# Kernel optimization log

Measured on AMD Instinct MI355X. Metric: run time of the kernel, lower is better.

## Reference

```python
import jax, jax.numpy as jnp
import numpy as np

D_MODEL = 192; D_INNER = 384; N_STATE = 16; D_CONV = 4; DT_RANK = 12; DEPTH = 24
PATCH = 16; STRIDE = 16; IMG = 128; EPS = 1e-5


def _ln(x, w, b):
    m = jnp.mean(x, -1, keepdims=True)
    v = jnp.mean((x - m) ** 2, -1, keepdims=True)
    return (x - m) * jax.lax.rsqrt(v + EPS) * w + b


def _mamba_dir(xz, cw, cb, xpw, dpw, dpb, Alog, Dv):
    # xz: (B, L, 2*d_inner); one direction of the bidirectional Mamba mixer
    xp, z = jnp.split(xz, 2, axis=-1)               # (B,L,di) each
    xc = jnp.transpose(xp, (0, 2, 1))               # (B,di,L)
    xc = jnp.pad(xc, ((0, 0), (0, 0), (D_CONV - 1, 0)))  # causal pad
    xc = jax.lax.conv_general_dilated(
        xc, cw, (1,), 'VALID',
        dimension_numbers=('NCH', 'OIH', 'NCH'),
        feature_group_count=D_INNER) + cb[None, :, None]
    u = jax.nn.silu(jnp.transpose(xc, (0, 2, 1)))   # (B,L,di)
    dbl = u @ xpw.T                                  # (B,L,dt_rank+2N)
    dt, Bm, Cm = jnp.split(dbl, [DT_RANK, DT_RANK + N_STATE], axis=-1)
    dt = jax.nn.softplus(dt @ dpw.T + dpb)           # (B,L,di)
    A = -jnp.exp(Alog)                               # (di,N)
    dA = jnp.exp(dt[..., None] * A)                  # (B,L,di,N)
    dBu = (dt * u)[..., None] * Bm[:, :, None, :]    # (B,L,di,N)

    def comb(c1, c2):
        a1, b1 = c1
        a2, b2 = c2
        return a1 * a2, a2 * b1 + b2

    _, h = jax.lax.associative_scan(comb, (dA, dBu), axis=1)
    y = jnp.einsum('bldn,bln->bld', h, Cm) + u * Dv
    return y * jax.nn.silu(z)


def _forward(x, patch_w, patch_b, ln_w, ln_b, in_w,
             cf_w, cf_b, xpf_w, dtf_w, dtf_b, Alog_f, D_f,
             cbk_w, cbk_b, xpb_w, dtb_w, dtb_b, Alog_b, D_b,
             out_w, nf_w, nf_b, head_w, head_b):
    B = x.shape[0]
    p = jax.lax.conv_general_dilated(
        x, patch_w, (STRIDE,) * 3, 'VALID',
        dimension_numbers=('NCDHW', 'OIDHW', 'NCDHW')) + patch_b[None, :, None, None, None]
    hidden = p.reshape(B, D_MODEL, -1).transpose(0, 2, 1)  # (B, L=512, D)
    residual = jnp.zeros_like(hidden)

    xs = (ln_w, ln_b, in_w, cf_w, cf_b, xpf_w, dtf_w, dtf_b, Alog_f, D_f,
          cbk_w, cbk_b, xpb_w, dtb_w, dtb_b, Alog_b, D_b, out_w)

    def step(carry, pl):
        hidden, residual = carry
        (lw, lb, iw, cfw, cfb, xpf, dwf, dbf, Af, Dfv,
         cbw, cbb, xpb, dwb, dbb, Ab, Dbv, ow) = pl
        residual = residual + hidden
        hn = _ln(residual, lw, lb)
        xz = hn @ iw.T                               # (B,L,2di)
        yf = _mamba_dir(xz, cfw, cfb, xpf, dwf, dbf, Af, Dfv)
        yb = jnp.flip(_mamba_dir(jnp.flip(xz, 1), cbw, cbb, xpb, dwb, dbb, Ab, Dbv), 1)
        hidden = (yf + yb) @ ow.T
        return (hidden, residual), None

    (hidden, residual), _ = jax.lax.scan(step, (hidden, residual), xs)
    final = _ln(residual + hidden, nf_w, nf_b)
    feat = final[:, -1, :]                           # final_pool_type='none' -> last token
    return feat @ head_w.T + head_b


def setup_inputs() -> dict:
    key = jax.random.key(0)
    ks = jax.random.split(key, 16)
    rn = lambda k, s, sc=0.02: jax.random.normal(k, s, jnp.float32) * sc
    d = {}
    d['x'] = jax.random.normal(ks[0], (1, 1, IMG, IMG, IMG), jnp.float32)
    d['patch_w'] = rn(ks[1], (D_MODEL, 1, PATCH, PATCH, PATCH), 0.05)
    d['patch_b'] = jnp.zeros((D_MODEL,), jnp.float32)
    d['ln_w'] = jnp.ones((DEPTH, D_MODEL), jnp.float32)
    d['ln_b'] = jnp.zeros((DEPTH, D_MODEL), jnp.float32)
    d['in_w'] = rn(ks[2], (DEPTH, 2 * D_INNER, D_MODEL))
    d['cf_w'] = rn(ks[3], (DEPTH, D_INNER, 1, D_CONV), 0.2)
    d['cf_b'] = jnp.zeros((DEPTH, D_INNER), jnp.float32)
    d['xpf_w'] = rn(ks[4], (DEPTH, DT_RANK + 2 * N_STATE, D_INNER))
    d['dtf_w'] = rn(ks[5], (DEPTH, D_INNER, DT_RANK), 0.1)
    d['dtf_b'] = jnp.full((DEPTH, D_INNER), -4.6, jnp.float32)  # softplus -> dt~0.01
    d['Alog_f'] = jnp.log(jnp.broadcast_to(jnp.arange(1, N_STATE + 1, dtype=jnp.float32), (DEPTH, D_INNER, N_STATE)))
    d['D_f'] = jnp.ones((DEPTH, D_INNER), jnp.float32)
    d['cbk_w'] = rn(ks[6], (DEPTH, D_INNER, 1, D_CONV), 0.2)
    d['cbk_b'] = jnp.zeros((DEPTH, D_INNER), jnp.float32)
    d['xpb_w'] = rn(ks[7], (DEPTH, DT_RANK + 2 * N_STATE, D_INNER))
    d['dtb_w'] = rn(ks[8], (DEPTH, D_INNER, DT_RANK), 0.1)
    d['dtb_b'] = jnp.full((DEPTH, D_INNER), -4.6, jnp.float32)
    d['Alog_b'] = jnp.log(jnp.broadcast_to(jnp.arange(1, N_STATE + 1, dtype=jnp.float32), (DEPTH, D_INNER, N_STATE)))
    d['D_b'] = jnp.ones((DEPTH, D_INNER), jnp.float32)
    d['out_w'] = rn(ks[9], (DEPTH, D_MODEL, D_INNER))
    d['nf_w'] = jnp.ones((D_MODEL,), jnp.float32)
    d['nf_b'] = jnp.zeros((D_MODEL,), jnp.float32)
    d['head_w'] = rn(ks[10], (2, D_MODEL))
    d['head_b'] = jnp.zeros((2,), jnp.float32)
    return d


def reference(x, patch_w, patch_b, ln_w, ln_b, in_w,
              cf_w, cf_b, xpf_w, dtf_w, dtf_b, Alog_f, D_f,
              cbk_w, cbk_b, xpb_w, dtb_w, dtb_b, Alog_b, D_b,
              out_w, nf_w, nf_b, head_w, head_b):
    return _forward(x, patch_w, patch_b, ln_w, ln_b, in_w,
                    cf_w, cf_b, xpf_w, dtf_w, dtf_b, Alog_f, D_f,
                    cbk_w, cbk_b, xpb_w, dtb_w, dtb_b, Alog_b, D_b,
                    out_w, nf_w, nf_b, head_w, head_b)
```

## Files before the change

kernel.cpp:

```cpp
#include <hip/hip_runtime.h>
#include <hip/hip_bf16.h>

#define D_MODEL 192
#define D_INNER 384
#define N_STATE 16
#define DT_RANK 12
#define DEPTH 24
#define SEQ 512
#define NCHUNK 8
#define CLEN 64
#define TS 68
#define AS 33
#define PART_STRIDE (SEQ * D_MODEL)
#define USTR (SEQ * D_INNER)
#define KSPLIT 16
#define NBLK 512
#define FSTR 32

typedef __hip_bfloat16 bf16;
typedef unsigned short u16;
typedef unsigned long long u64;

__device__ __forceinline__ float silu_f(float x) { return x / (1.f + __expf(-x)); }
__device__ __forceinline__ float softplus_f(float x) {
    return (x > 20.f) ? x : log1pf(__expf(x));
}
__device__ __forceinline__ float bf2f(unsigned u) {
    return __uint_as_float(u << 16);
}
__device__ __forceinline__ u16 f2bu(float f) {
    bf16 b = __float2bfloat16(f);
    return *reinterpret_cast<u16*>(&b);
}

__device__ __forceinline__ float aload(const float* p) {
    return __hip_atomic_load(p, __ATOMIC_RELAXED, __HIP_MEMORY_SCOPE_AGENT);
}
__device__ __forceinline__ void astore(float* p, float v) {
    __hip_atomic_store(p, v, __ATOMIC_RELAXED, __HIP_MEMORY_SCOPE_AGENT);
}
__device__ __forceinline__ unsigned aloadu(const unsigned* p) {
    return __hip_atomic_load(p, __ATOMIC_RELAXED, __HIP_MEMORY_SCOPE_AGENT);
}
__device__ __forceinline__ void astoreu(unsigned* p, unsigned v) {
    __hip_atomic_store(p, v, __ATOMIC_RELAXED, __HIP_MEMORY_SCOPE_AGENT);
}
__device__ __forceinline__ float2 aload2(const float* p) {
    const u64 v = __hip_atomic_load((const u64*)p, __ATOMIC_RELAXED, __HIP_MEMORY_SCOPE_AGENT);
    return make_float2(__uint_as_float((unsigned)v), __uint_as_float((unsigned)(v >> 32)));
}
__device__ __forceinline__ void astore2(float* p, float x, float y) {
    const u64 v = (u64)__float_as_uint(x) | ((u64)__float_as_uint(y) << 32);
    __hip_atomic_store((u64*)p, v, __ATOMIC_RELAXED, __HIP_MEMORY_SCOPE_AGENT);
}
__device__ __forceinline__ float4 aload4v(const float* p) {
    const float2 a = aload2(p), b = aload2(p + 2);
    return make_float4(a.x, a.y, b.x, b.y);
}
__device__ __forceinline__ void astore4v(float* p, float4 v) {
    astore2(p, v.x, v.y); astore2(p + 2, v.z, v.w);
}

template<typename T> __device__ __forceinline__ float ld(const void* p, long i) {
    return ((const float*)p)[i];
}
template<> __device__ __forceinline__ float ld<bf16>(const void* p, long i) {
    return bf2f(((const u16*)p)[i]);
}
template<typename T> __device__ __forceinline__ float4 ld4(const void* p, long i) {
    return *(const float4*)((const float*)p + i);
}
template<> __device__ __forceinline__ float4 ld4<bf16>(const void* p, long i) {
    const ushort4 v = *(const ushort4*)((const u16*)p + i);
    return make_float4(bf2f(v.x), bf2f(v.y), bf2f(v.z), bf2f(v.w));
}
template<typename T> __device__ __forceinline__ void st(void* p, int i, float v) {
    ((float*)p)[i] = v;
}
template<> __device__ __forceinline__ void st<bf16>(void* p, int i, float v) {
    ((bf16*)p)[i] = __float2bfloat16(v);
}
__device__ __forceinline__ float dot4(const float4& a, const float4& b) {
    return a.x * b.x + a.y * b.y + a.z * b.z + a.w * b.w;
}
__device__ __forceinline__ void ld8b(const u16* p, float4& a, float4& b) {
    const uint4 u = *(const uint4*)p;
    a.x = bf2f(u.x & 0xffffu); a.y = bf2f(u.x >> 16);
    a.z = bf2f(u.y & 0xffffu); a.w = bf2f(u.y >> 16);
    b.x = bf2f(u.z & 0xffffu); b.y = bf2f(u.z >> 16);
    b.z = bf2f(u.w & 0xffffu); b.w = bf2f(u.w >> 16);
}
__device__ __forceinline__ float4 ld4b(const u16* p) {
    const uint2 u = *(const uint2*)p;
    return make_float4(bf2f(u.x & 0xffffu), bf2f(u.x >> 16),
                       bf2f(u.y & 0xffffu), bf2f(u.y >> 16));
}

__device__ __forceinline__ void gbar(unsigned* bar, unsigned target, bool fence) {
    asm volatile("s_waitcnt vmcnt(0)" ::: "memory");
    __syncthreads();
    const int bid = blockIdx.x, tid = threadIdx.x;
    unsigned* gen0 = bar + 512 * FSTR;
    if (tid == 0) {
        if (fence) __threadfence();
        astoreu(&bar[bid * FSTR], target);
    }
    if (bid == 0) {
        int spins = 0;
        for (;;) {
            const unsigned va = aloadu(&bar[tid * FSTR]);
            const unsigned vb = aloadu(&bar[(tid + 256) * FSTR]);
            const bool ok = (va >= target) && (vb >= target);
            if (__syncthreads_and(ok)) break;
            if (++spins > (1 << 20)) break;
            __builtin_amdgcn_s_sleep(1);
        }
        if (tid == 0) astoreu(gen0, target);
    } else if (tid == 0) {
        int spins = 0;
        if (bid < 16) {
            while (aloadu(gen0) < target) {
                if (++spins > (1 << 20)) break;
                __builtin_amdgcn_s_sleep(2);
            }
            astoreu(&gen0[bid * FSTR], target);
        } else if (bid < 32) {
            while (aloadu(gen0) < target) {
                if (++spins > (1 << 20)) break;
                __builtin_amdgcn_s_sleep(2);
            }
        } else {
            unsigned* rl = &gen0[(bid >> 5) * FSTR];
            while (aloadu(rl) < target) {
                if (++spins > (1 << 20)) break;
                __builtin_amdgcn_s_sleep(2);
            }
        }
    }
    if (fence && tid == 0) __threadfence();
    __syncthreads();
}

__device__ void cvtB(const void* s, u16* d, long n, long g, long str, int isb) {
    if (isb) {
        const u16* p = (const u16*)s;
        for (long i = g * 4; i < n; i += str * 4) *(ushort4*)(d + i) = *(const ushort4*)(p + i);
    } else {
        const float* p = (const float*)s;
        for (long i = g * 4; i < n; i += str * 4) {
            const float4 v = *(const float4*)(p + i);
            ushort4 o; o.x = f2bu(v.x); o.y = f2bu(v.y); o.z = f2bu(v.z); o.w = f2bu(v.w);
            *(ushort4*)(d + i) = o;
        }
    }
}
__device__ void cvtF(const void* s, float* d, long n, long g, long str, int isb) {
    if (isb) {
        const u16* p = (const u16*)s;
        for (long i = g * 4; i < n; i += str * 4) {
            const ushort4 v = *(const ushort4*)(p + i);
            *(float4*)(d + i) = make_float4(bf2f(v.x), bf2f(v.y), bf2f(v.z), bf2f(v.w));
        }
    } else {
        const float* p = (const float*)s;
        for (long i = g * 4; i < n; i += str * 4) *(float4*)(d + i) = *(const float4*)(p + i);
    }
}
__device__ void cvtNA(const void* s, float* d, long n, long g, long str, int isb) {
    if (isb) {
        const u16* p = (const u16*)s;
        for (long i = g * 4; i < n; i += str * 4) {
            const ushort4 v = *(const ushort4*)(p + i);
            *(float4*)(d + i) = make_float4(-__expf(bf2f(v.x)), -__expf(bf2f(v.y)),
                                            -__expf(bf2f(v.z)), -__expf(bf2f(v.w)));
        }
    } else {
        const float* p = (const float*)s;
        for (long i = g * 4; i < n; i += str * 4) {
            const float4 v = *(const float4*)(p + i);
            *(float4*)(d + i) = make_float4(-__expf(v.x), -__expf(v.y), -__expf(v.z), -__expf(v.w));
        }
    }
}

template<typename T>
__device__ void final_phase(int tid, const float* res, const float* y, const void* ow,
                            const void* nw, const void* nb, const void* hw, const void* hb,
                            void* out, float* syf, float* f, float* red) {
    for (int i = tid; i < D_INNER; i += 256)
        syf[i] = aload(&y[(long)511 * D_INNER + i]) + aload(&y[(long)USTR + 511 * D_INNER + i]);
    __syncthreads();
    float v = 0.f;
    if (tid < D_MODEL) {
        float acc = 0.f;
        const long wrow = (long)(DEPTH - 1) * D_MODEL * D_INNER + (long)tid * D_INNER;
        for (int k = 0; k < D_INNER; k += 4)
            acc += dot4(ld4<T>(ow, wrow + k), *(const float4*)&syf[k]);
        v = aload(&res[511 * D_MODEL + tid]) + acc;
    }
    float s = v;
    #pragma unroll
    for (int o = 32; o > 0; o >>= 1) s += __shfl_down(s, o, 64);
    if ((tid & 63) == 0 && tid < D_MODEL) red[tid >> 6] = s;
    __syncthreads();
    const float mean = (red[0] + red[1] + red[2]) * (1.f / D_MODEL);
    const float d = (tid < D_MODEL) ? (v - mean) : 0.f;
    float s2 = d * d;
    #pragma unroll
    for (int o = 32; o > 0; o >>= 1) s2 += __shfl_down(s2, o, 64);
    if ((tid & 63) == 0 && tid < D_MODEL) red[3 + (tid >> 6)] = s2;
    __syncthreads();
    const float var = (red[3] + red[4] + red[5]) * (1.f / D_MODEL);
    if (tid < D_MODEL)
        f[tid] = d * rsqrtf(var + 1e-5f) * ld<T>(nw, tid) + ld<T>(nb, tid);
    __syncthreads();
    if (tid < 2) {
        float a2 = ld<T>(hb, tid);
        for (int c = 0; c < D_MODEL; ++c) a2 += f[c] * ld<T>(hw, tid * D_MODEL + c);
        st<T>(out, tid, a2);
    }
}

struct MegaArgs {
    const void *x, *pw, *pb, *lnw, *lnb, *inw, *cfw, *cfb, *xpfw, *dtfw, *dtfb, *Af, *Dfv;
    const void *cbw, *cbb, *xpbw, *dtbw, *dtbb, *Ab, *Dbv, *ow, *nfw, *nfb, *hw, *hb;
    void* out;
    unsigned* bar;
    float *hidC, *res0, *res1, *xz, *u, *dbl, *dt, *y, *chunkH, *chunkP;
    float *lnwF, *lnbF, *cbfF, *cbbF, *dtbfF, *dtbbF, *negAfF, *negAbF, *DfF, *DbF, *pbF;
    u16 *inwB, *owB, *xB, *pwB, *xpwfB, *xpwbB, *dtwfB, *dtwbB, *cwfB, *cwbB;
};

__global__ void init_kernel(unsigned* bar) {
    const int i = blockIdx.x * 256 + threadIdx.x;
    ((uint4*)bar)[i] = make_uint4(0, 0, 0, 0);
}

__global__ void __launch_bounds__(256, 2) mega_kernel(MegaArgs a) {
    __shared__ float smem[6144];
    const int bid = blockIdx.x;
    const int tid = threadIdx.x;
    unsigned* bar = a.bar;
    unsigned* scanR = a.bar + 528 * FSTR;
    unsigned gen_ctr = 0;
    const int isb = (((const unsigned*)a.lnw)[0] != 0x3F800000u);

    {
        const long g = (long)bid * 256 + tid;
        const long str = (long)NBLK * 256;
        cvtB(a.inw,  a.inwB,  3538944, g, str, isb);
        cvtB(a.ow,   a.owB,   1769472, g, str, isb);
        cvtB(a.x,    a.xB,    2097152, g, str, isb);
        cvtB(a.pw,   a.pwB,    786432, g, str, isb);
        cvtB(a.xpfw, a.xpwfB,  405504, g, str, isb);
        cvtB(a.xpbw, a.xpwbB,  405504, g, str, isb);
        cvtB(a.dtfw, a.dtwfB,  110592, g, str, isb);
        cvtB(a.dtbw, a.dtwbB,  110592, g, str, isb);
        cvtB(a.cfw,  a.cwfB,    36864, g, str, isb);
        cvtB(a.cbw,  a.cwbB,    36864, g, str, isb);
        cvtF(a.lnw,  a.lnwF,     4608, g, str, isb);
        cvtF(a.lnb,  a.lnbF,     4608, g, str, isb);
        cvtF(a.cfb,  a.cbfF,     9216, g, str, isb);
        cvtF(a.cbb,  a.cbbF,     9216, g, str, isb);
        cvtF(a.dtfb, a.dtbfF,    9216, g, str, isb);
        cvtF(a.dtbb, a.dtbbF,    9216, g, str, isb);
        cvtF(a.pb,   a.pbF,       192, g, str, isb);
        cvtNA(a.Af,  a.negAfF,  147456, g, str, isb);
        cvtNA(a.Ab,  a.negAbF,  147456, g, str, isb);
        cvtF(a.Dfv,  a.DfF,      9216, g, str, isb);
        cvtF(a.Dbv,  a.DbF,      9216, g, str, isb);
    }
    gbar(bar, ++gen_ctr, true);

    {
        float* As_ = smem;
        float* Ws  = smem + 1056;
        const int ty = tid >> 4, tx = tid & 15;
        for (int unit = bid; unit < 768; unit += NBLK) {
            const int mt = unit & 15, nt = (unit >> 4) % 3, ks = unit / 48;
            const int m0 = mt * 32, n0 = nt * 64, kk0 = ks * 256;
            float acc[2][4] = {};
            for (int kk = kk0; kk < kk0 + 256; kk += 32) {
                for (int e = tid; e < 1024; e += 256) {
                    const int m = e >> 5, k = e & 31;
                    const int kid = kk + k, t = m0 + m;
                    const int dz = kid >> 8, dy = (kid >> 4) & 15, dx = kid & 15;
                    const int pz = t >> 6, py = (t >> 3) & 7, px = t & 7;
                    As_[k * AS + m] = bf2f(a.xB[(long)(pz * 16 + dz) * 16384 + (py * 16 + dy) * 128 + (px * 16 + dx)]);
                }
                for (int e = tid; e < 2048; e += 256) {
                    const int n = e >> 5, k = e & 31;
                    Ws[k * TS + n] = bf2f(a.pwB[(long)(n0 + n) * 4096 + kk + k]);
                }
                __syncthreads();
                #pragma unroll 8
                for (int k = 0; k < 32; ++k) {
                    const float a0 = As_[k * AS + ty * 2];
                    const float a1 = As_[k * AS + ty * 2 + 1];
                    const float4 w4 = *(const float4*)&Ws[k * TS + tx * 4];
                    acc[0][0] += a0 * w4.x; acc[0][1] += a0 * w4.y;
                    acc[0][2] += a0 * w4.z; acc[0][3] += a0 * w4.w;
                    acc[1][0] += a1 * w4.x; acc[1][1] += a1 * w4.y;
                    acc[1][2] += a1 * w4.z; acc[1][3] += a1 * w4.w;
                }
                __syncthreads();
            }
            float* C = a.hidC + (long)ks * PART_STRIDE;
            #pragma unroll
            for (int i = 0; i < 2; ++i) {
                float4 o4 = make_float4(acc[i][0], acc[i][1], acc[i][2], acc[i][3]);
                if (ks == 0) {
                    o4.x += a.pbF[n0 + tx * 4 + 0];
                    o4.y += a.pbF[n0 + tx * 4 + 1];
                    o4.z += a.pbF[n0 + tx * 4 + 2];
                    o4.w += a.pbF[n0 + tx * 4 + 3];
                }
                astore4v(&C[(m0 + ty * 2 + i) * D_MODEL + n0 + tx * 4], o4);
            }
        }
    }
    gbar(bar, ++gen_ctr, false);

    const int ch = tid >> 4, np = tid & 15;
    float* sU  = smem;
    float* sDT = smem + 1024;
    float* sBC = smem + 2048;
    float* sZ  = smem + 4096;
    float* sY  = smem + 5120;

    for (int l = 0; l < DEPTH; ++l) {
        const int first = (l == 0);
        const float* resIn = (l & 1) ? a.res1 : a.res0;
        float* resOut      = (l & 1) ? a.res0 : a.res1;

        if (bid < 256) {
            float* sy  = smem;
            float* lnS = smem + 768;
            float* hnS = smem + 1152;
            const int t0 = bid * 2;
            if (!first) {
                for (int j = tid; j < 384; j += 256) {
                    const int tt = j / 192, d2 = (j - tt * 192) * 2;
                    const long o = (long)(t0 + tt) * D_INNER + d2;
                    const float2 v1 = aload2(&a.y[o]);
                    const float2 v2 = aload2(&a.y[(long)USTR + o]);
                    sy[tt * D_INNER + d2]     = v1.x + v2.x;
                    sy[tt * D_INNER + d2 + 1] = v1.y + v2.y;
                }
            }
            __syncthreads();
            if (tid < D_MODEL) {
                float accB[2];
                if (first) {
                    #pragma unroll
                    for (int tt = 0; tt < 2; ++tt) {
                        float s = 0.f;
                        #pragma unroll
                        for (int sp = 0; sp < KSPLIT; ++sp)
                            s += aload(&a.hidC[(long)sp * PART_STRIDE + (t0 + tt) * D_MODEL + tid]);
                        accB[tt] = s;
                    }
                } else {
                    accB[0] = accB[1] = 0.f;
                    const u16* wr = a.owB + (long)(l - 1) * D_MODEL * D_INNER + (long)tid * D_INNER;
                    for (int k = 0; k < D_INNER; k += 8) {
                        float4 va, vb;
                        ld8b(wr + k, va, vb);
                        accB[0] += dot4(va, *(const float4*)&sy[k]) + dot4(vb, *(const float4*)&sy[k + 4]);
                        accB[1] += dot4(va, *(const float4*)&sy[D_INNER + k]) + dot4(vb, *(const float4*)&sy[D_INNER + k + 4]);
                    }
                }
                #pragma unroll
                for (int tt = 0; tt < 2; ++tt) {
                    const float rv = accB[tt] + (first ? 0.f : aload(&resIn[(t0 + tt) * D_MODEL + tid]));
                    lnS[tt * D_MODEL + tid] = rv;
                    astore(&resOut[(t0 + tt) * D_MODEL + tid], rv);
                }
            }
            __syncthreads();
            {
                const int w = tid >> 6, lane = tid & 63;
                if (w < 2) {
                    const float v0 = lnS[w * D_MODEL + lane];
                    const float v1 = lnS[w * D_MODEL + lane + 64];
                    const float v2 = lnS[w * D_MODEL + lane + 128];
                    float s = v0 + v1 + v2;
                    #pragma unroll
                    for (int o = 32; o > 0; o >>= 1) s += __shfl_xor(s, o, 64);
                    const float mean = s * (1.f / D_MODEL);
                    const float d0 = v0 - mean, d1 = v1 - mean, d2 = v2 - mean;
                    float s2 = d0 * d0 + d1 * d1 + d2 * d2;
                    #pragma unroll
                    for (int o = 32; o > 0; o >>= 1) s2 += __shfl_xor(s2, o, 64);
                    const float rstd = rsqrtf(s2 * (1.f / D_MODEL) + 1e-5f);
                    hnS[w * D_MODEL + lane]       = d0 * rstd * a.lnwF[l * D_MODEL + lane]       + a.lnbF[l * D_MODEL + lane];
                    hnS[w * D_MODEL + lane + 64]  = d1 * rstd * a.lnwF[l * D_MODEL + lane + 64]  + a.lnbF[l * D_MODEL + lane + 64];
                    hnS[w * D_MODEL + lane + 128] = d2 * rstd * a.lnwF[l * D_MODEL + lane + 128] + a.lnbF[l * D_MODEL + lane + 128];
                }
            }
            __syncthreads();
            float accD[3][2] = {};
            const u16* w0 = a.inwB + (long)l * 2 * D_INNER * D_MODEL;
            for (int k = 0; k < D_MODEL; k += 8) {
                #pragma unroll
                for (int r = 0; r < 3; ++r) {
                    float4 va, vb;
                    ld8b(w0 + (long)(tid + r * 256) * D_MODEL + k, va, vb);
                    #pragma unroll
                    for (int tt = 0; tt < 2; ++tt) {
                        accD[r][tt] += dot4(va, *(const float4*)&hnS[tt * D_MODEL + k])
                                     + dot4(vb, *(const float4*)&hnS[tt * D_MODEL + k + 4]);
                    }
                }
            }
            #pragma unroll
            for (int r = 0; r < 3; ++r)
                #pragma unroll
                for (int tt = 0; tt < 2; ++tt)
                    astore(&a.xz[(long)(t0 + tt) * 2 * D_INNER + tid + r * 256], accD[r][tt]);
        }
        gbar(bar, ++gen_ctr, false);

        {
            float* su   = smem;
            float* dblP = smem + 768;
            float* dblS = smem + 960;
            const int dir = bid >> 8;
            const u16* cwB   = dir ? a.cwbB  : a.cwfB;
            const float* cbF = dir ? a.cbbF  : a.cbfF;
            const u16* xpwB  = dir ? a.xpwbB : a.xpwfB;
            const u16* dtwB  = dir ? a.dtwbB : a.dtwfB;
            const float* dtbF = dir ? a.dtbbF : a.dtbfF;
            const int t0 = (bid & 255) * 2;
            float* ub = a.u + (long)dir * USTR;
            for (int j = tid; j < 384; j += 256) {
                const int tt = j / 192, d2 = (j - tt * 192) * 2;
                const int t = t0 + tt;
                float4 wa, wb;
                ld8b(cwB + (long)(l * D_INNER + d2) * 4, wa, wb);
                const float cw0[4] = {wa.x, wa.y, wa.z, wa.w};
                const float cw1[4] = {wb.x, wb.y, wb.z, wb.w};
                float acc0 = cbF[l * D_INNER + d2];
                float acc1 = cbF[l * D_INNER + d2 + 1];
                #pragma unroll
                for (int k = 0; k < 4; ++k) {
                    const int ii = t + k - 3;
                    if (ii >= 0) {
                        const int src = dir ? (511 - ii) : ii;
                        const float2 xv = aload2(&a.xz[(long)src * 2 * D_INNER + d2]);
                        acc0 += xv.x * cw0[k];
                        acc1 += xv.y * cw1[k];
                    }
                }
                const float u0 = silu_f(acc0), u1 = silu_f(acc1);
                su[tt * D_INNER + d2] = u0;
                su[tt * D_INNER + d2 + 1] = u1;
                astore2(&ub[(long)t * D_INNER + d2], u0, u1);
            }
            __syncthreads();
            if (tid < 176) {
                const int half = tid / 88;
                const int r = tid - half * 88;
                const int tt = r / 44, out = r - tt * 44;
                const u16* wr = xpwB + (long)(l * 44 + out) * D_INNER;
                const int k0 = half * 192;
                float acc = 0.f;
                for (int k = k0; k < k0 + 192; k += 8) {
                    float4 va, vb;
                    ld8b(wr + k, va, vb);
                    acc += dot4(va, *(const float4*)&su[tt * D_INNER + k])
                         + dot4(vb, *(const float4*)&su[tt * D_INNER + k + 4]);
                }
                dblP[half * 96 + tt * 48 + out] = acc;
            }
            __syncthreads();
            if (tid < 88) {
                const int tt = tid / 44, out = tid - tt * 44;
                const float s = dblP[tt * 48 + out] + dblP[96 + tt * 48 + out];
                dblS[tt * 48 + out] = s;
                astore(&a.dbl[(long)dir * SEQ * 44 + (long)(t0 + tt) * 44 + out], s);
            }
            __syncthreads();
            float* dtp = a.dt + (long)dir * USTR;
            for (int j = tid; j < 384; j += 256) {
                const int tt = j / 192, d2 = (j - tt * 192) * 2;
                const u16* wr = dtwB + (long)(l * D_INNER + d2) * DT_RANK;
                float4 A0, B0; ld8b(wr, A0, B0);
                const float4 C0 = ld4b(wr + 8);
                float4 A1, B1; ld8b(wr + 12, A1, B1);
                const float4 C1 = ld4b(wr + 20);
                const float* ds = &dblS[tt * 48];
                const float4 ds0 = *(const float4*)ds;
                const float4 ds1 = *(const float4*)(ds + 4);
                const float4 ds2 = *(const float4*)(ds + 8);
                const float acc0 = dtbF[l * D_INNER + d2]
                    + dot4(A0, ds0) + dot4(B0, ds1) + dot4(C0, ds2);
                const float acc1 = dtbF[l * D_INNER + d2 + 1]
                    + dot4(A1, ds0) + dot4(B1, ds1) + dot4(C1, ds2);
                astore2(&dtp[(long)(t0 + tt) * D_INNER + d2],
                        softplus_f(acc0), softplus_f(acc1));
            }
        }
        gbar(bar, ++gen_ctr, false);

        if (bid < 384) {
            const int dg = bid % 24, chunk = (bid / 24) & 7, dir2 = bid / 192;
            const int d0 = dg * 16, d = d0 + ch;
            const int t0s = chunk * CLEN;
            const float* ub  = a.u  + (long)dir2 * USTR;
            const float* dtp = a.dt + (long)dir2 * USTR;
            const float* db  = a.dbl + (long)dir2 * SEQ * 44;
            {
                const int t = tid >> 2, dl4 = (tid & 3) * 4;
                const int tg = t0s + t;
                const long base = (long)tg * D_INNER + d0 + dl4;
                *(float4*)&sU[t * 16 + dl4]  = aload4v(&ub[base]);
                *(float4*)&sDT[t * 16 + dl4] = aload4v(&dtp[base]);
                const int out_l = dir2 ? (511 - tg) : tg;
                *(float4*)&sZ[t * 16 + dl4] = aload4v(&a.xz[(long)out_l * 2 * D_INNER + D_INNER + d0 + dl4]);
            }
            for (int i = tid; i < 512; i += 256) {
                const int t = i >> 3, j4 = (i & 7) * 4;
                *(float4*)&sBC[t * 32 + j4] = aload4v(&db[(long)(t0s + t) * 44 + DT_RANK + j4]);
            }
            const float* negA = dir2 ? a.negAbF : a.negAfF;
            const float Areg = negA[(long)(l * D_INNER + d) * N_STATE + np];
            const float Dval = (dir2 ? a.DbF : a.DfF)[l * D_INNER + d];
            __syncthreads();
            float h = 0.f, dts = 0.f;
            for (int t = 0; t < CLEN; ++t) {
                const float dtv = sDT[t * 16 + ch];
                h = __expf(dtv * Areg) * h + (dtv * sU[t * 16 + ch]) * sBC[t * 32 + np];
                dts += dtv;
            }
            const long cb = ((long)(dir2 * NCHUNK + chunk) * D_INNER + d) * N_STATE + np;
            astore(&a.chunkH[cb], h);
            astore(&a.chunkP[cb], __expf(Areg * dts));
            asm volatile("s_waitcnt vmcnt(0)" ::: "memory");
            __syncthreads();
            if (tid == 0)
                astoreu(&scanR[((dir2 * NCHUNK + chunk) * 24 + dg) * FSTR], (unsigned)(l + 1));
            if (tid < chunk) {
                unsigned* fl = &scanR[((dir2 * NCHUNK + tid) * 24 + dg) * FSTR];
                int spins = 0;
                while (aloadu(fl) < (unsigned)(l + 1)) {
                    if (++spins > (1 << 20)) break;
                    __builtin_amdgcn_s_sleep(1);
                }
            }
            __syncthreads();
            float hs[NCHUNK - 1], ps[NCHUNK - 1];
            #pragma unroll
            for (int c = 0; c < NCHUNK - 1; ++c) {
                if (c < chunk) {
                    const long cbb = ((long)(dir2 * NCHUNK + c) * D_INNER + d) * N_STATE + np;
                    hs[c] = aload(&a.chunkH[cbb]);
                    ps[c] = aload(&a.chunkP[cbb]);
                }
            }
            float h0 = 0.f;
            #pragma unroll
            for (int c = 0; c < NCHUNK - 1; ++c)
                if (c < chunk) h0 = ps[c] * h0 + hs[c];
            h = h0;
            for (int t = 0; t < CLEN; ++t) {
                const float dtv = sDT[t * 16 + ch];
                const float uv = sU[t * 16 + ch];
                h = __expf(dtv * Areg) * h + (dtv * uv) * sBC[t * 32 + np];
                float part = h * sBC[t * 32 + 16 + np];
                part += __shfl_xor(part, 1, 64);
                part += __shfl_xor(part, 2, 64);
                part += __shfl_xor(part, 4, 64);
                part += __shfl_xor(part, 8, 64);
                if (np == 0)
                    sY[t * 16 + ch] = (part + uv * Dval) * silu_f(sZ[t * 16 + ch]);
            }
            __syncthreads();
            {
                const int t = tid >> 2, dl4 = (tid & 3) * 4;
                const int tg = t0s + t;
                const int out_l = dir2 ? (511 - tg) : tg;
                float* yb = a.y + (long)dir2 * USTR;
                astore4v(&yb[(long)out_l * D_INNER + d0 + dl4], *(float4*)&sY[t * 16 + dl4]);
            }
        }
        gbar(bar, ++gen_ctr, false);
    }

    if (bid == 0) {
        float* syf = smem;
        float* f   = smem + 384;
        float* red = smem + 576;
        if (isb) final_phase<bf16>(tid, a.res0, a.y, a.ow, a.nfw, a.nfb, a.hw, a.hb, a.out, syf, f, red);
        else     final_phase<float>(tid, a.res0, a.y, a.ow, a.nfw, a.nfb, a.hw, a.hb, a.out, syf, f, red);
    }
}

extern "C" void kernel_launch(void* const* d_in, const int* in_sizes, int n_in,
                              void* d_out, int out_size, void* d_ws, size_t ws_size,
                              hipStream_t stream) {
    (void)in_sizes; (void)n_in; (void)out_size; (void)ws_size;
    const void* x    = d_in[0];
    const void* pw   = d_in[1];
    const void* pb   = d_in[2];
    const void* lnw  = d_in[3];
    const void* lnb  = d_in[4];
    const void* inw  = d_in[5];
    const void* cfw  = d_in[6];
    const void* cfb  = d_in[7];
    const void* xpfw = d_in[8];
    const void* dtfw = d_in[9];
    const void* dtfb = d_in[10];
    const void* Af   = d_in[11];
    const void* Dfv  = d_in[12];
    const void* cbw  = d_in[13];
    const void* cbb  = d_in[14];
    const void* xpbw = d_in[15];
    const void* dtbw = d_in[16];
    const void* dtbb = d_in[17];
    const void* Ab   = d_in[18];
    const void* Dbv  = d_in[19];
    const void* ow   = d_in[20];
    const void* nfw  = d_in[21];
    const void* nfb  = d_in[22];
    const void* hw   = d_in[23];
    const void* hb   = d_in[24];

    unsigned* bar = (unsigned*)d_ws;
    float* w = (float*)((char*)d_ws + 131072);
    float* hidC   = w;  w += KSPLIT * PART_STRIDE;
    float* res0   = w;  w += PART_STRIDE;
    float* res1   = w;  w += PART_STRIDE;
    float* xz     = w;  w += SEQ * 2 * D_INNER;
    float* u      = w;  w += 2 * USTR;
    float* dbl    = w;  w += 2 * SEQ * 44;
    float* dt     = w;  w += 2 * USTR;
    float* y      = w;  w += 2 * USTR;
    float* chunkH = w;  w += 2 * NCHUNK * D_INNER * N_STATE;
    float* chunkP = w;  w += 2 * NCHUNK * D_INNER * N_STATE;
    float* lnwF = w;  w += 4608;
    float* lnbF = w;  w += 4608;
    float* cbfF = w;  w += 9216;
    float* cbbF = w;  w += 9216;
    float* dtbfF = w; w += 9216;
    float* dtbbF = w; w += 9216;
    float* negAfF = w; w += 147456;
    float* negAbF = w; w += 147456;
    float* DfF = w;   w += 9216;
    float* DbF = w;   w += 9216;
    float* pbF = w;   w += 192;
    u16* b = (u16*)w;
    u16* inwB  = b;  b += 3538944;
    u16* owB   = b;  b += 1769472;
    u16* xB    = b;  b += 2097152;
    u16* pwB   = b;  b += 786432;
    u16* xpwfB = b;  b += 405504;
    u16* xpwbB = b;  b += 405504;
    u16* dtwfB = b;  b += 110592;
    u16* dtwbB = b;  b += 110592;
    u16* cwfB  = b;  b += 36864;
    u16* cwbB  = b;  b += 36864;

    MegaArgs ma;
    ma.x = x; ma.pw = pw; ma.pb = pb; ma.lnw = lnw; ma.lnb = lnb; ma.inw = inw;
    ma.cfw = cfw; ma.cfb = cfb; ma.xpfw = xpfw; ma.dtfw = dtfw; ma.dtfb = dtfb;
    ma.Af = Af; ma.Dfv = Dfv; ma.cbw = cbw; ma.cbb = cbb; ma.xpbw = xpbw;
    ma.dtbw = dtbw; ma.dtbb = dtbb; ma.Ab = Ab; ma.Dbv = Dbv; ma.ow = ow;
    ma.nfw = nfw; ma.nfb = nfb; ma.hw = hw; ma.hb = hb; ma.out = d_out;
    ma.bar = bar;
    ma.hidC = hidC; ma.res0 = res0; ma.res1 = res1; ma.xz = xz; ma.u = u;
    ma.dbl = dbl; ma.dt = dt; ma.y = y; ma.chunkH = chunkH; ma.chunkP = chunkP;
    ma.lnwF = lnwF; ma.lnbF = lnbF; ma.cbfF = cbfF; ma.cbbF = cbbF;
    ma.dtbfF = dtbfF; ma.dtbbF = dtbbF; ma.negAfF = negAfF; ma.negAbF = negAbF;
    ma.DfF = DfF; ma.DbF = DbF; ma.pbF = pbF;
    ma.inwB = inwB; ma.owB = owB; ma.xB = xB; ma.pwB = pwB;
    ma.xpwfB = xpwfB; ma.xpwbB = xpwbB; ma.dtwfB = dtwfB; ma.dtwbB = dtwbB;
    ma.cwfB = cwfB; ma.cwbB = cwbB;

    init_kernel<<<32, 256, 0, stream>>>(bar);
    mega_kernel<<<NBLK, 256, 0, stream>>>(ma);
}
```

Before: 2.049 ms.

## Replace two grid barriers per layer with producer-consumer flags

Two full-grid barriers per layer are replaced with per-block flags. Stage 2 blocks wait only on the stage-1 blocks that produced the xz rows their causal convolution reads, and the scan blocks wait only on the 32 stage-2 blocks covering their chunk. This removes the global synchronisation stalls in each of the 24 layers and lets stages overlap. In exchange it adds flag memory, moves the workspace offset and zeroes a larger init region, and correctness depends on the dependency ranges being exactly right.

```diff
diff --git a/kernel.cpp b/kernel.cpp
--- a/kernel.cpp
+++ b/kernel.cpp
@@ -94,6 +94,19 @@
     const uint2 u = *(const uint2*)p;
     return make_float4(bf2f(u.x & 0xffffu), bf2f(u.x >> 16),
                        bf2f(u.y & 0xffffu), bf2f(u.y >> 16));
+}
+
+__device__ __forceinline__ void post_flag(unsigned* fl, unsigned v, int tid) {
+    asm volatile("s_waitcnt vmcnt(0)" ::: "memory");
+    __syncthreads();
+    if (tid == 0) astoreu(fl, v);
+}
+__device__ __forceinline__ void wait_flag(const unsigned* fl, unsigned v) {
+    int spins = 0;
+    while (aloadu(fl) < v) {
+        if (++spins > (1 << 20)) break;
+        __builtin_amdgcn_s_sleep(1);
+    }
 }
 
 __device__ __forceinline__ void gbar(unsigned* bar, unsigned target, bool fence) {
@@ -242,6 +255,8 @@
     const int tid = threadIdx.x;
     unsigned* bar = a.bar;
     unsigned* scanR = a.bar + 528 * FSTR;
+    unsigned* aflag = a.bar + 912 * FSTR;
+    unsigned* bflag = a.bar + 1168 * FSTR;
     unsigned gen_ctr = 0;
     const int isb = (((const unsigned*)a.lnw)[0] != 0x3F800000u);
 
@@ -330,6 +345,7 @@
 
     for (int l = 0; l < DEPTH; ++l) {
         const int first = (l == 0);
+        const unsigned lv = (unsigned)(l + 1);
         const float* resIn = (l & 1) ? a.res1 : a.res0;
         float* resOut      = (l & 1) ? a.res0 : a.res1;
 
@@ -418,20 +434,27 @@
                 #pragma unroll
                 for (int tt = 0; tt < 2; ++tt)
                     astore(&a.xz[(long)(t0 + tt) * 2 * D_INNER + tid + r * 256], accD[r][tt]);
-        }
-        gbar(bar, ++gen_ctr, false);
+            post_flag(&aflag[bid * FSTR], lv, tid);
+        }
 
         {
+            const int dir = bid >> 8, bb = bid & 255;
+            int lo, hi;
+            if (dir == 0) { lo = bb >= 2 ? bb - 2 : 0; hi = bb; }
+            else { lo = bb <= 255 ? (255 - bb > 0 ? 255 - bb : 0) : 0;
+                   hi = 257 - bb <= 255 ? 257 - bb : 255; }
+            if (tid <= hi - lo) wait_flag(&aflag[(lo + tid) * FSTR], lv);
+            __syncthreads();
+
             float* su   = smem;
             float* dblP = smem + 768;
             float* dblS = smem + 960;
-            const int dir = bid >> 8;
             const u16* cwB   = dir ? a.cwbB  : a.cwfB;
             const float* cbF = dir ? a.cbbF  : a.cbfF;
             const u16* xpwB  = dir ? a.xpwbB : a.xpwfB;
             const u16* dtwB  = dir ? a.dtwbB : a.dtwfB;
             const float* dtbF = dir ? a.dtbbF : a.dtbfF;
-            const int t0 = (bid & 255) * 2;
+            const int t0 = bb * 2;
             float* ub = a.u + (long)dir * USTR;
             for (int j = tid; j < 384; j += 256) {
                 const int tt = j / 192, d2 = (j - tt * 192) * 2;
@@ -500,11 +523,13 @@
                 astore2(&dtp[(long)(t0 + tt) * D_INNER + d2],
                         softplus_f(acc0), softplus_f(acc1));
             }
-        }
-        gbar(bar, ++gen_ctr, false);
+            post_flag(&bflag[bid * FSTR], lv, tid);
+        }
 
         if (bid < 384) {
             const int dg = bid % 24, chunk = (bid / 24) & 7, dir2 = bid / 192;
+            if (tid < 32) wait_flag(&bflag[(dir2 * 256 + chunk * 32 + tid) * FSTR], lv);
+            __syncthreads();
             const int d0 = dg * 16, d = d0 + ch;
             const int t0s = chunk * CLEN;
             const float* ub  = a.u  + (long)dir2 * USTR;
@@ -536,18 +561,8 @@
             const long cb = ((long)(dir2 * NCHUNK + chunk) * D_INNER + d) * N_STATE + np;
             astore(&a.chunkH[cb], h);
             astore(&a.chunkP[cb], __expf(Areg * dts));
-            asm volatile("s_waitcnt vmcnt(0)" ::: "memory");
-            __syncthreads();
-            if (tid == 0)
-                astoreu(&scanR[((dir2 * NCHUNK + chunk) * 24 + dg) * FSTR], (unsigned)(l + 1));
-            if (tid < chunk) {
-                unsigned* fl = &scanR[((dir2 * NCHUNK + tid) * 24 + dg) * FSTR];
-                int spins = 0;
-                while (aloadu(fl) < (unsigned)(l + 1)) {
-                    if (++spins > (1 << 20)) break;
-                    __builtin_amdgcn_s_sleep(1);
-                }
-            }
+            post_flag(&scanR[((dir2 * NCHUNK + chunk) * 24 + dg) * FSTR], lv, tid);
+            if (tid < chunk) wait_flag(&scanR[((dir2 * NCHUNK + tid) * 24 + dg) * FSTR], lv);
             __syncthreads();
             float hs[NCHUNK - 1], ps[NCHUNK - 1];
             #pragma unroll
@@ -627,7 +642,7 @@
     const void* hb   = d_in[24];
 
     unsigned* bar = (unsigned*)d_ws;
-    float* w = (float*)((char*)d_ws + 131072);
+    float* w = (float*)((char*)d_ws + 262144);
     float* hidC   = w;  w += KSPLIT * PART_STRIDE;
     float* res0   = w;  w += PART_STRIDE;
     float* res1   = w;  w += PART_STRIDE;
@@ -677,6 +692,6 @@
     ma.xpwfB = xpwfB; ma.xpwbB = xpwbB; ma.dtwfB = dtwfB; ma.dtwbB = dtwbB;
     ma.cwfB = cwfB; ma.cwbB = cwbB;
 
-    init_kernel<<<32, 256, 0, stream>>>(bar);
+    init_kernel<<<64, 256, 0, stream>>>(bar);
     mega_kernel<<<NBLK, 256, 0, stream>>>(ma);
 }
```

After: 1.955 ms. -4.6%, faster.
